# Performance work log

Measured on AMD Instinct MI355X. Metric: run time of the kernel, lower is better.

The kernel has to match this reference:

```python
import jax, jax.numpy as jnp
import numpy as np

B, L, E = 16, 1022, 1280
D, H, FF, NL = 512, 8, 2048, 4
DH = D // H
EPS = 1e-5


def layer_norm(x, s, b):
    m = jnp.mean(x, axis=-1, keepdims=True)
    v = jnp.mean(jnp.square(x - m), axis=-1, keepdims=True)
    return (x - m) * jax.lax.rsqrt(v + EPS) * s + b


def setup_inputs() -> dict:
    key = jax.random.key(0)
    ks = jax.random.split(key, 12)
    s = 0.02
    return {
        "embeddings": jax.random.normal(ks[0], (B, L, E), jnp.float32),
        "mask": jnp.ones((B, L), jnp.float32),
        "position": jnp.tile(jnp.arange(L, dtype=jnp.int32)[None, :], (B, 1)),
        "proj_w": jax.random.normal(ks[1], (D, E), jnp.float32) * s,
        "proj_b": jnp.zeros((D,), jnp.float32),
        "proj_ln_s": jnp.ones((D,), jnp.float32),
        "proj_ln_b": jnp.zeros((D,), jnp.float32),
        "ln1_s": jnp.ones((NL, D), jnp.float32),
        "ln1_b": jnp.zeros((NL, D), jnp.float32),
        "in_w": jax.random.normal(ks[2], (NL, 3 * D, D), jnp.float32) * s,
        "in_b": jnp.zeros((NL, 3 * D), jnp.float32),
        "out_w": jax.random.normal(ks[3], (NL, D, D), jnp.float32) * s,
        "out_b": jnp.zeros((NL, D), jnp.float32),
        "ln2_s": jnp.ones((NL, D), jnp.float32),
        "ln2_b": jnp.zeros((NL, D), jnp.float32),
        "w1": jax.random.normal(ks[4], (NL, FF, D), jnp.float32) * s,
        "b1": jnp.zeros((NL, FF), jnp.float32),
        "w2": jax.random.normal(ks[5], (NL, D, FF), jnp.float32) * s,
        "b2": jnp.zeros((NL, D), jnp.float32),
        "h1_w": jax.random.normal(ks[6], (128, 2 * D), jnp.float32) * s,
        "h1_b": jnp.zeros((128,), jnp.float32),
        "hln_s": jnp.ones((128,), jnp.float32),
        "hln_b": jnp.zeros((128,), jnp.float32),
        "h2_w": jax.random.normal(ks[7], (1, 128), jnp.float32) * s,
        "h2_b": jnp.zeros((1,), jnp.float32),
    }


def _rope_tables():
    inv_freq = 1.0 / (10000.0 ** (jnp.arange(0, DH, 2, dtype=jnp.float32) / DH))
    t = jnp.arange(L, dtype=jnp.float32)
    freqs = jnp.outer(t, inv_freq)          # [L, DH/2]
    emb = jnp.concatenate([freqs, freqs], axis=-1)  # [L, DH]
    return jnp.cos(emb), jnp.sin(emb)


def _rotate_half(x):
    x1, x2 = jnp.split(x, 2, axis=-1)
    return jnp.concatenate([-x2, x1], axis=-1)


def _apply_rope(x, cos, sin):
    # x: [B, L, D] -> per-head rotation -> [B, L, D]
    xh = x.reshape(B, L, H, DH)
    xh = xh * cos[None, :, None, :] + _rotate_half(xh) * sin[None, :, None, :]
    return xh.reshape(B, L, D)


def _forward(embeddings, mask, proj_w, proj_b, proj_ln_s, proj_ln_b,
             ln1_s, ln1_b, in_w, in_b, out_w, out_b, ln2_s, ln2_b,
             w1, b1, w2, b2, h1_w, h1_b, hln_s, hln_b, h2_w, h2_b):
    cos, sin = _rope_tables()
    x = layer_norm(embeddings @ proj_w.T + proj_b, proj_ln_s, proj_ln_b)  # [B,L,D]
    pad = mask <= 0  # True where padded (~mask.bool())
    scale = 1.0 / jnp.sqrt(jnp.float32(DH))
    for i in range(NL):
        n = layer_norm(x, ln1_s[i], ln1_b[i])
        q_in = _apply_rope(n, cos, sin)
        k_in = _apply_rope(n, cos, sin)
        v_in = n
        wq, wk, wv = jnp.split(in_w[i], 3, axis=0)
        bq, bk, bv = jnp.split(in_b[i], 3, axis=0)
        qh = (q_in @ wq.T + bq).reshape(B, L, H, DH)
        kh = (k_in @ wk.T + bk).reshape(B, L, H, DH)
        vh = (v_in @ wv.T + bv).reshape(B, L, H, DH)
        scores = jnp.einsum('blhd,bmhd->bhlm', qh, kh) * scale
        scores = jnp.where(pad[:, None, None, :], jnp.float32(-1e9), scores)
        attn = jax.nn.softmax(scores, axis=-1)
        o = jnp.einsum('bhlm,bmhd->blhd', attn, vh).reshape(B, L, D)
        x = x + (o @ out_w[i].T + out_b[i])
        n2 = layer_norm(x, ln2_s[i], ln2_b[i])
        x = x + (jax.nn.relu(n2 @ w1[i].T + b1[i]) @ w2[i].T + b2[i])
    # masked mean pool
    gctx = (x * mask[..., None]).sum(axis=1) / mask.sum(axis=1, keepdims=True)  # [B,D]
    combined = jnp.concatenate([x, jnp.broadcast_to(gctx[:, None, :], (B, L, D))], axis=-1)
    h = jax.nn.relu(layer_norm(combined @ h1_w.T + h1_b, hln_s, hln_b))
    logits = (h @ h2_w.T + h2_b).squeeze(-1)  # [B,L]
    return logits


def reference(embeddings, mask, position, proj_w, proj_b, proj_ln_s, proj_ln_b,
              ln1_s, ln1_b, in_w, in_b, out_w, out_b, ln2_s, ln2_b,
              w1, b1, w2, b2, h1_w, h1_b, hln_s, hln_b, h2_w, h2_b):
    # position is accepted for API parity but unused (as in the torch module)
    return _forward(embeddings, mask, proj_w, proj_b, proj_ln_s, proj_ln_b,
                    ln1_s, ln1_b, in_w, in_b, out_w, out_b, ln2_s, ln2_b,
                    w1, b1, w2, b2, h1_w, h1_b, hln_s, hln_b, h2_w, h2_b)
```

## Files before the change

kernel.cpp:

```cpp
#include <hip/hip_runtime.h>
#include <cstdint>
#include <cstddef>

#define B_   16
#define L_   1022
#define E_   1280
#define D_   512
#define H_   8
#define FF_  2048
#define NL_  4
#define DH_  64
#define BL_  (B_*L_)
#define EPS_ 1e-5f

typedef unsigned short u16;
typedef unsigned int   u32;
typedef unsigned long long u64;
typedef float f32x4 __attribute__((ext_vector_type(4)));
typedef short s16x8 __attribute__((ext_vector_type(8)));
typedef u32 u32x4 __attribute__((ext_vector_type(4)));

__device__ __forceinline__ u16 f2bf(float f) {
    u32 u = __builtin_bit_cast(u32, f);
    u += 0x7fffu + ((u >> 16) & 1u);
    return (u16)(u >> 16);
}
__device__ __forceinline__ float bf2f(u16 u) {
    return __builtin_bit_cast(float, (u32)u << 16);
}
__device__ __forceinline__ u32 pack2bf(float a, float b) {
    return (u32)f2bf(a) | ((u32)f2bf(b) << 16);
}

__global__ __launch_bounds__(256)
void cast_k(const float* __restrict__ src, u16* __restrict__ dst, int n8) {
    int t = blockIdx.x * 256 + threadIdx.x;
    if (t >= n8) return;
    const float* s = src + (size_t)t * 8;
    float4 a = *(const float4*)(s);
    float4 b = *(const float4*)(s + 4);
    s16x8 o;
    o[0] = (short)f2bf(a.x); o[1] = (short)f2bf(a.y);
    o[2] = (short)f2bf(a.z); o[3] = (short)f2bf(a.w);
    o[4] = (short)f2bf(b.x); o[5] = (short)f2bf(b.y);
    o[6] = (short)f2bf(b.z); o[7] = (short)f2bf(b.w);
    *(s16x8*)(dst + (size_t)t * 8) = o;
}

__global__ __launch_bounds__(256)
void h1cast_k(const float* __restrict__ src, u16* __restrict__ dst) {
    int t = blockIdx.x * 256 + threadIdx.x;
    if (t >= 128 * 512 / 8) return;
    int row = t >> 6, c8 = (t & 63) << 3;
    const float* s = src + (size_t)row * 1024 + c8;
    float4 a = *(const float4*)(s);
    float4 b = *(const float4*)(s + 4);
    s16x8 o;
    o[0] = (short)f2bf(a.x); o[1] = (short)f2bf(a.y);
    o[2] = (short)f2bf(a.z); o[3] = (short)f2bf(a.w);
    o[4] = (short)f2bf(b.x); o[5] = (short)f2bf(b.y);
    o[6] = (short)f2bf(b.z); o[7] = (short)f2bf(b.w);
    *(s16x8*)(dst + (size_t)row * 512 + c8) = o;
}

__global__ void tables_k(float* __restrict__ ct, float* __restrict__ st) {
    int idx = blockIdx.x * blockDim.x + threadIdx.x;
    if (idx >= L_ * DH_) return;
    int l = idx / DH_;
    int d = idx % DH_;
    int j = d & 31;
    float invf = powf(10000.0f, -(float)(2 * j) / (float)DH_);
    float ang = (float)l * invf;
    ct[idx] = cosf(ang);
    st[idx] = sinf(ang);
}

template<bool RELU, bool RESID, bool OUTBF, bool ROWBIAS>
__global__ __launch_bounds__(256)
void mgemm_k(const u16* __restrict__ A, const u16* __restrict__ W,
             const float* __restrict__ bias, const float* __restrict__ resid,
             void* __restrict__ Cout, int M, int N, int K)
{
    constexpr int LDT = 72;
    __shared__ u16 As[128 * LDT];
    __shared__ u16 Ws[128 * LDT];
    const int nt = N >> 7;
    const int bx = blockIdx.x % nt;
    const int by = blockIdx.x / nt;
    const int m0 = by << 7, n0 = bx << 7;
    const int tid = threadIdx.x;
    const int lane = tid & 63, wid = tid >> 6;
    const int wr = wid >> 1, wc = wid & 1;
    const int lr = lane & 15, lk = lane >> 4;

    f32x4 acc[4][4];
#pragma unroll
    for (int m = 0; m < 4; m++)
#pragma unroll
        for (int n = 0; n < 4; n++) acc[m][n] = (f32x4)0.0f;

    for (int k0 = 0; k0 < K; k0 += 64) {
        s16x8 va[4], vw[4];
#pragma unroll
        for (int u = 0; u < 4; u++) {
            int ch = tid + (u << 8);
            int r = ch >> 3, c8 = (ch & 7) << 3;
            int ar = m0 + r; if (ar >= M) ar = M - 1;
            va[u] = *(const s16x8*)(A + (size_t)ar * K + k0 + c8);
            vw[u] = *(const s16x8*)(W + (size_t)(n0 + r) * K + k0 + c8);
        }
        __syncthreads();
#pragma unroll
        for (int u = 0; u < 4; u++) {
            int ch = tid + (u << 8);
            int r = ch >> 3, c8 = (ch & 7) << 3;
            *(s16x8*)&As[r * LDT + c8] = va[u];
            *(s16x8*)&Ws[r * LDT + c8] = vw[u];
        }
        __syncthreads();
#pragma unroll
        for (int kk = 0; kk < 2; kk++) {
            s16x8 af[4], bf[4];
#pragma unroll
            for (int m = 0; m < 4; m++)
                af[m] = *(const s16x8*)&As[(wr * 64 + m * 16 + lr) * LDT + kk * 32 + lk * 8];
#pragma unroll
            for (int n = 0; n < 4; n++)
                bf[n] = *(const s16x8*)&Ws[(wc * 64 + n * 16 + lr) * LDT + kk * 32 + lk * 8];
#pragma unroll
            for (int m = 0; m < 4; m++)
#pragma unroll
                for (int n = 0; n < 4; n++)
                    acc[m][n] = __builtin_amdgcn_mfma_f32_16x16x32_bf16(
                        af[m], bf[n], acc[m][n], 0, 0, 0);
        }
    }

    float bv[4];
    if constexpr (!ROWBIAS) {
#pragma unroll
        for (int n = 0; n < 4; n++) bv[n] = bias[n0 + wc * 64 + n * 16 + lr];
    }
#pragma unroll
    for (int m = 0; m < 4; m++) {
#pragma unroll
        for (int j = 0; j < 4; j++) {
            int row = m0 + wr * 64 + m * 16 + lk * 4 + j;
            if (row >= M) continue;
            const float* rb = nullptr;
            if constexpr (ROWBIAS) rb = bias + (size_t)(row / L_) * N;
#pragma unroll
            for (int n = 0; n < 4; n++) {
                int col = n0 + wc * 64 + n * 16 + lr;
                float c = acc[m][n][j];
                if constexpr (ROWBIAS) c += rb[col];
                else                   c += bv[n];
                if constexpr (RELU) c = fmaxf(c, 0.0f);
                if constexpr (RESID) c += resid[(size_t)row * N + col];
                if constexpr (OUTBF) ((u16*)Cout)[(size_t)row * N + col] = f2bf(c);
                else                 ((float*)Cout)[(size_t)row * N + col] = c;
            }
        }
    }
}

template<int DD, bool RELU, bool OUTBF>
__global__ __launch_bounds__(256)
void ln_k(const float* __restrict__ x, const float* __restrict__ s,
          const float* __restrict__ bb, void* __restrict__ out, int M)
{
    const int lane = threadIdx.x & 63;
    const int row = (blockIdx.x << 2) + (threadIdx.x >> 6);
    if (row >= M) return;
    const float* xr = x + (size_t)row * DD;
    constexpr int NV = DD / 64;
    float v[NV];
    if constexpr (NV == 8) {
        *(float4*)(v)     = *(const float4*)(xr + lane * 8);
        *(float4*)(v + 4) = *(const float4*)(xr + lane * 8 + 4);
    } else {
        float2 t = *(const float2*)(xr + lane * 2);
        v[0] = t.x; v[1] = t.y;
    }
    float sum = 0.f, sq = 0.f;
#pragma unroll
    for (int e = 0; e < NV; e++) { sum += v[e]; sq += v[e] * v[e]; }
#pragma unroll
    for (int msk = 1; msk < 64; msk <<= 1) {
        sum += __shfl_xor(sum, msk);
        sq  += __shfl_xor(sq, msk);
    }
    const float mean = sum * (1.0f / DD);
    const float var  = sq * (1.0f / DD) - mean * mean;
    const float rstd = rsqrtf(var + EPS_);
#pragma unroll
    for (int e = 0; e < NV; e++) {
        int d = lane * NV + e;
        float r = (v[e] - mean) * rstd * s[d] + bb[d];
        if constexpr (RELU) r = fmaxf(r, 0.0f);
        v[e] = r;
    }
    if constexpr (OUTBF) {
        u16* orow = (u16*)out + (size_t)row * DD;
        if constexpr (NV == 8) {
            s16x8 o;
#pragma unroll
            for (int e = 0; e < 8; e++) o[e] = (short)f2bf(v[e]);
            *(s16x8*)(orow + lane * 8) = o;
        } else {
            orow[lane * 2] = f2bf(v[0]); orow[lane * 2 + 1] = f2bf(v[1]);
        }
    } else {
        float* orow = (float*)out + (size_t)row * DD;
        if constexpr (NV == 8) {
            *(float4*)(orow + lane * 8)     = *(float4*)(v);
            *(float4*)(orow + lane * 8 + 4) = *(float4*)(v + 4);
        } else {
            float2 t; t.x = v[0]; t.y = v[1];
            *(float2*)(orow + lane * 2) = t;
        }
    }
}

__global__ __launch_bounds__(256)
void rope_k(const u16* __restrict__ n, const float* __restrict__ ct,
            const float* __restrict__ st, u16* __restrict__ r)
{
    int t = blockIdx.x * 256 + threadIdx.x;
    if (t >= BL_ * D_ / 8) return;
    int idx = t << 3;
    int l = (idx / D_) % L_;
    int d = idx & (D_ - 1);
    int dd = d & 63;
    s16x8 xv = *(const s16x8*)(n + idx);
    int pidx; float sgn;
    if (dd < 32) { pidx = idx + 32; sgn = -1.0f; }
    else         { pidx = idx - 32; sgn =  1.0f; }
    s16x8 pv = *(const s16x8*)(n + pidx);
    float4 c0 = *(const float4*)(ct + l * DH_ + dd);
    float4 c1 = *(const float4*)(ct + l * DH_ + dd + 4);
    float4 s0 = *(const float4*)(st + l * DH_ + dd);
    float4 s1 = *(const float4*)(st + l * DH_ + dd + 4);
    float cc[8] = {c0.x,c0.y,c0.z,c0.w,c1.x,c1.y,c1.z,c1.w};
    float ss[8] = {s0.x,s0.y,s0.z,s0.w,s1.x,s1.y,s1.z,s1.w};
    s16x8 o;
#pragma unroll
    for (int e = 0; e < 8; e++) {
        float xf = bf2f((u16)xv[e]);
        float pf = bf2f((u16)pv[e]);
        o[e] = (short)f2bf(xf * cc[e] + sgn * pf * ss[e]);
    }
    *(s16x8*)(r + idx) = o;
}

__global__ __launch_bounds__(256)
void attn_k(const u16* __restrict__ qk, const u16* __restrict__ v,
            const float* __restrict__ mask, u16* __restrict__ o)
{
    constexpr int LDA = 68;
    __shared__ u16 Kt[64 * LDA];
    __shared__ u16 Vt[64 * LDA];
    const int bh = blockIdx.x >> 4, qt = blockIdx.x & 15;
    const int b = bh >> 3, h = bh & 7;
    const int tid = threadIdx.x;
    const int lane = tid & 63, w = tid >> 6;
    const int lr = lane & 15, lg = lane >> 4;
    const size_t basebl = (size_t)b * L_;

    const int qrow = qt * 64 + w * 16 + lr;
    const int qc = qrow < L_ ? qrow : L_ - 1;
    s16x8 bq[2];
#pragma unroll
    for (int kk = 0; kk < 2; kk++)
        bq[kk] = *(const s16x8*)(qk + (basebl + qc) * 1024 + h * DH_ + kk * 32 + lg * 8);

    f32x4 oacc[4];
#pragma unroll
    for (int n = 0; n < 4; n++) oacc[n] = (f32x4)0.0f;
    float m_run = -1e30f, l_run = 0.f;

    const int st_key = tid >> 3;
    const int st_d8 = (tid & 7) << 3;
    const int src0 = lr + ((lane & 16) << 1);
    const int src1 = src0 + 16;
    const bool ahi = (lg >> 1) != 0;

    for (int kt = 0; kt < 16; kt++) {
        __syncthreads();
#pragma unroll
        for (int u = 0; u < 2; u++) {
            int key = st_key + u * 32;
            int gk = kt * 64 + key; if (gk >= L_) gk = L_ - 1;
            s16x8 kv = *(const s16x8*)(qk + (basebl + gk) * 1024 + 512 + h * DH_ + st_d8);
            s16x8 vv = *(const s16x8*)(v  + (basebl + gk) * D_ + h * DH_ + st_d8);
            *(s16x8*)&Kt[key * LDA + st_d8] = kv;
#pragma unroll
            for (int e = 0; e < 8; e++) Vt[(st_d8 + e) * LDA + key] = (u16)vv[e];
        }
        __syncthreads();

        int gkey = kt * 64 + lane;
        bool vb = (gkey < L_) && (mask[basebl + gkey] > 0.0f);
        u64 vm = __ballot(vb);

        f32x4 sacc[4];
#pragma unroll
        for (int n = 0; n < 4; n++) {
            sacc[n] = (f32x4)0.0f;
#pragma unroll
            for (int kk = 0; kk < 2; kk++) {
                s16x8 ak = *(const s16x8*)&Kt[(n * 16 + lr) * LDA + kk * 32 + lg * 8];
                sacc[n] = __builtin_amdgcn_mfma_f32_16x16x32_bf16(ak, bq[kk], sacc[n], 0, 0, 0);
            }
        }

        float p[4][4];
        float tm = -1e30f;
#pragma unroll
        for (int n = 0; n < 4; n++)
#pragma unroll
            for (int j = 0; j < 4; j++) {
                int kl = 16 * n + 4 * lg + j;
                float s = ((vm >> kl) & 1ull) ? sacc[n][j] * 0.125f : -1e30f;
                p[n][j] = s;
                tm = fmaxf(tm, s);
            }
        tm = fmaxf(tm, __shfl_xor(tm, 16));
        tm = fmaxf(tm, __shfl_xor(tm, 32));
        float nm = fmaxf(m_run, tm);
        float corr = __expf(m_run - nm);
        m_run = nm;
        float ts = 0.f;
#pragma unroll
        for (int n = 0; n < 4; n++)
#pragma unroll
            for (int j = 0; j < 4; j++) {
                p[n][j] = __expf(p[n][j] - nm);
                ts += p[n][j];
            }
        ts += __shfl_xor(ts, 16);
        ts += __shfl_xor(ts, 32);
        l_run = l_run * corr + ts;
#pragma unroll
        for (int n = 0; n < 4; n++) oacc[n] *= corr;

        u32 pk[4][2];
#pragma unroll
        for (int n = 0; n < 4; n++) {
            pk[n][0] = pack2bf(p[n][0], p[n][1]);
            pk[n][1] = pack2bf(p[n][2], p[n][3]);
        }
        u32 r0[4][2], r1[4][2];
#pragma unroll
        for (int n = 0; n < 4; n++)
#pragma unroll
            for (int i = 0; i < 2; i++) {
                r0[n][i] = (u32)__shfl((int)pk[n][i], src0);
                r1[n][i] = (u32)__shfl((int)pk[n][i], src1);
            }
#pragma unroll
        for (int kk = 0; kk < 2; kk++) {
            u32x4 bw;
            bw[0] = ahi ? r0[2 * kk + 1][0] : r0[2 * kk][0];
            bw[1] = ahi ? r0[2 * kk + 1][1] : r0[2 * kk][1];
            bw[2] = ahi ? r1[2 * kk + 1][0] : r1[2 * kk][0];
            bw[3] = ahi ? r1[2 * kk + 1][1] : r1[2 * kk][1];
            s16x8 bp = __builtin_bit_cast(s16x8, bw);
#pragma unroll
            for (int n2 = 0; n2 < 4; n2++) {
                s16x8 av = *(const s16x8*)&Vt[(n2 * 16 + lr) * LDA + kk * 32 + lg * 8];
                oacc[n2] = __builtin_amdgcn_mfma_f32_16x16x32_bf16(av, bp, oacc[n2], 0, 0, 0);
            }
        }
    }

    __syncthreads();
    u16* Ol = &Kt[w * 16 * LDA];
    float inv = 1.0f / l_run;
#pragma unroll
    for (int n = 0; n < 4; n++)
#pragma unroll
        for (int j = 0; j < 4; j++)
            Ol[lr * LDA + 16 * n + 4 * lg + j] = f2bf(oacc[n][j] * inv);
    int orow = lane >> 2, oc = (lane & 3) * 16;
    int qg = qt * 64 + w * 16 + orow;
    if (qg < L_) {
        s16x8 o0 = *(const s16x8*)&Ol[orow * LDA + oc];
        s16x8 o1 = *(const s16x8*)&Ol[orow * LDA + oc + 8];
        *(s16x8*)(o + (basebl + qg) * D_ + h * DH_ + oc) = o0;
        *(s16x8*)(o + (basebl + qg) * D_ + h * DH_ + oc + 8) = o1;
    }
}

__global__ __launch_bounds__(512)
void pool1_k(const float* __restrict__ x, const float* __restrict__ mask,
             float* __restrict__ pp, float* __restrict__ mp)
{
    const int b = blockIdx.x, sp = blockIdx.y;
    const int d = threadIdx.x;
    const int l0 = sp * 64;
    float acc = 0.f;
    for (int l = l0; l < l0 + 64 && l < L_; l++)
        acc += x[((size_t)b * L_ + l) * D_ + d] * mask[b * L_ + l];
    pp[((size_t)b * 16 + sp) * D_ + d] = acc;
    if (d == 0) {
        float ms = 0.f;
        for (int l = l0; l < l0 + 64 && l < L_; l++) ms += mask[b * L_ + l];
        mp[b * 16 + sp] = ms;
    }
}

__global__ __launch_bounds__(512)
void pool2_k(const float* __restrict__ pp, const float* __restrict__ mp,
             float* __restrict__ g)
{
    const int b = blockIdx.x;
    const int d = threadIdx.x;
    float acc = 0.f, ms = 0.f;
#pragma unroll
    for (int sp = 0; sp < 16; sp++) {
        acc += pp[((size_t)b * 16 + sp) * D_ + d];
        ms += mp[b * 16 + sp];
    }
    g[b * D_ + d] = acc / ms;
}

__global__ __launch_bounds__(256)
void gpart_k(const float* __restrict__ g, const float* __restrict__ h1w,
             const float* __restrict__ h1b, float* __restrict__ gp)
{
    const int lane = threadIdx.x & 63;
    const int gid = (blockIdx.x << 2) + (threadIdx.x >> 6);
    const int b = gid >> 7, j = gid & 127;
    const float* wr = h1w + (size_t)j * (2 * D_) + D_;
    const float* gr = g + b * D_;
    float4 a0 = *(const float4*)(gr + lane * 8);
    float4 a1 = *(const float4*)(gr + lane * 8 + 4);
    float4 w0 = *(const float4*)(wr + lane * 8);
    float4 w1v = *(const float4*)(wr + lane * 8 + 4);
    float acc = a0.x * w0.x + a0.y * w0.y + a0.z * w0.z + a0.w * w0.w
              + a1.x * w1v.x + a1.y * w1v.y + a1.z * w1v.z + a1.w * w1v.w;
#pragma unroll
    for (int msk = 1; msk < 64; msk <<= 1) acc += __shfl_xor(acc, msk);
    if (lane == 0) gp[b * 128 + j] = acc + h1b[j];
}

__global__ __launch_bounds__(256)
void logits_k(const float* __restrict__ h, const float* __restrict__ w,
              const float* __restrict__ bsc, float* __restrict__ out, int M)
{
    const int lane = threadIdx.x & 63;
    const int row = (blockIdx.x << 2) + (threadIdx.x >> 6);
    if (row >= M) return;
    float2 hv = *(const float2*)(h + (size_t)row * 128 + lane * 2);
    float2 wv = *(const float2*)(w + lane * 2);
    float acc = hv.x * wv.x + hv.y * wv.y;
#pragma unroll
    for (int msk = 1; msk < 64; msk <<= 1) acc += __shfl_xor(acc, msk);
    if (lane == 0) out[row] = acc + bsc[0];
}

extern "C" void kernel_launch(void* const* d_in, const int* in_sizes, int n_in,
                              void* d_out, int out_size, void* d_ws, size_t ws_size,
                              hipStream_t stream)
{
    const float* emb       = (const float*)d_in[0];
    const float* mask      = (const float*)d_in[1];
    const float* proj_w    = (const float*)d_in[3];
    const float* proj_b    = (const float*)d_in[4];
    const float* proj_ln_s = (const float*)d_in[5];
    const float* proj_ln_b = (const float*)d_in[6];
    const float* ln1_s     = (const float*)d_in[7];
    const float* ln1_b     = (const float*)d_in[8];
    const float* in_w      = (const float*)d_in[9];
    const float* in_b      = (const float*)d_in[10];
    const float* out_w     = (const float*)d_in[11];
    const float* out_b     = (const float*)d_in[12];
    const float* ln2_s     = (const float*)d_in[13];
    const float* ln2_b     = (const float*)d_in[14];
    const float* w1        = (const float*)d_in[15];
    const float* b1        = (const float*)d_in[16];
    const float* w2        = (const float*)d_in[17];
    const float* b2        = (const float*)d_in[18];
    const float* h1_w      = (const float*)d_in[19];
    const float* h1_b      = (const float*)d_in[20];
    const float* hln_s     = (const float*)d_in[21];
    const float* hln_b     = (const float*)d_in[22];
    const float* h2_w      = (const float*)d_in[23];
    const float* h2_b      = (const float*)d_in[24];
    float* out = (float*)d_out;

    float* ws = (float*)d_ws;
    const size_t S = (size_t)BL_ * D_;
    float* X  = ws;
    float* Rf = ws + S;
    u16* QKB   = (u16*)(ws + S);
    u16* VB    = (u16*)(ws + 2 * S);
    u16* NbB   = (u16*)(ws + 2 * S) + S;
    u16* FFb16 = (u16*)(ws + 3 * S);
    u16* RopeB = FFb16;
    u16* embB  = FFb16;
    u16* RB    = (u16*)(ws + 4 * S);
    u16* projwB = (u16*)(ws + 5 * S);
    u16* iwB  = projwB + 512 * 1280;
    u16* owB  = iwB + (size_t)NL_ * 3 * D_ * D_;
    u16* w1B  = owB + (size_t)NL_ * D_ * D_;
    u16* w2B  = w1B + (size_t)NL_ * FF_ * D_;
    u16* h1wB = w2B + (size_t)NL_ * D_ * FF_;
    float* CT = ws + 5 * S + 6651904;
    float* ST = CT + L_ * DH_;
    float* GC = ST + L_ * DH_;
    float* GP = GC + B_ * D_;
    float* Pp = GP + B_ * 128;
    float* Mp = Pp + (size_t)B_ * 16 * D_;
    float* Hb = Rf;

    const int MT = 128;
    const dim3 blk(256);
    const int lnGrid = (BL_ + 3) / 4;

    cast_k<<<(BL_ * E_ / 8 + 255) / 256, blk, 0, stream>>>(emb, embB, BL_ * E_ / 8);
    cast_k<<<(512 * 1280 / 8 + 255) / 256, blk, 0, stream>>>(proj_w, projwB, 512 * 1280 / 8);
    cast_k<<<(NL_ * 3 * D_ * D_ / 8 + 255) / 256, blk, 0, stream>>>(in_w, iwB, NL_ * 3 * D_ * D_ / 8);
    cast_k<<<(NL_ * D_ * D_ / 8 + 255) / 256, blk, 0, stream>>>(out_w, owB, NL_ * D_ * D_ / 8);
    cast_k<<<(NL_ * FF_ * D_ / 8 + 255) / 256, blk, 0, stream>>>(w1, w1B, NL_ * FF_ * D_ / 8);
    cast_k<<<(NL_ * D_ * FF_ / 8 + 255) / 256, blk, 0, stream>>>(w2, w2B, NL_ * D_ * FF_ / 8);
    h1cast_k<<<(128 * 512 / 8 + 255) / 256, blk, 0, stream>>>(h1_w, h1wB);
    tables_k<<<(L_ * DH_ + 255) / 256, blk, 0, stream>>>(CT, ST);

    mgemm_k<false,false,false,false><<<MT * (D_ / 128), blk, 0, stream>>>(
        embB, projwB, proj_b, nullptr, Rf, BL_, D_, E_);
    ln_k<D_,false,false><<<lnGrid, blk, 0, stream>>>(Rf, proj_ln_s, proj_ln_b, X, BL_);

    for (int i = 0; i < NL_; i++) {
        const u16* iw = iwB + (size_t)i * 3 * D_ * D_;
        const float* ib = in_b + (size_t)i * 3 * D_;
        ln_k<D_,false,true><<<lnGrid, blk, 0, stream>>>(X, ln1_s + i * D_, ln1_b + i * D_, NbB, BL_);
        mgemm_k<false,false,true,false><<<MT * 4, blk, 0, stream>>>(
            NbB, iw + 2 * D_ * D_, ib + 2 * D_, nullptr, VB, BL_, D_, D_);
        rope_k<<<(BL_ * D_ / 8 + 255) / 256, blk, 0, stream>>>(NbB, CT, ST, RopeB);
        mgemm_k<false,false,true,false><<<MT * 8, blk, 0, stream>>>(
            RopeB, iw, ib, nullptr, QKB, BL_, 1024, D_);
        attn_k<<<B_ * H_ * 16, blk, 0, stream>>>(QKB, VB, mask, RB);
        mgemm_k<false,true,false,false><<<MT * 4, blk, 0, stream>>>(
            RB, owB + (size_t)i * D_ * D_, out_b + i * D_, X, X, BL_, D_, D_);
        ln_k<D_,false,true><<<lnGrid, blk, 0, stream>>>(X, ln2_s + i * D_, ln2_b + i * D_, NbB, BL_);
        mgemm_k<true,false,true,false><<<MT * 16, blk, 0, stream>>>(
            NbB, w1B + (size_t)i * FF_ * D_, b1 + i * FF_, nullptr, FFb16, BL_, FF_, D_);
        mgemm_k<false,true,false,false><<<MT * 4, blk, 0, stream>>>(
            FFb16, w2B + (size_t)i * D_ * FF_, b2 + i * D_, X, X, BL_, D_, FF_);
    }

    pool1_k<<<dim3(B_, 16), dim3(512), 0, stream>>>(X, mask, Pp, Mp);
    pool2_k<<<B_, dim3(512), 0, stream>>>(Pp, Mp, GC);
    gpart_k<<<(B_ * 128) / 4, blk, 0, stream>>>(GC, h1_w, h1_b, GP);
    cast_k<<<(int)((S / 8 + 255) / 256), blk, 0, stream>>>(X, NbB, (int)(S / 8));
    mgemm_k<false,false,false,true><<<MT * 1, blk, 0, stream>>>(
        NbB, h1wB, GP, nullptr, Hb, BL_, 128, D_);
    ln_k<128,true,false><<<lnGrid, blk, 0, stream>>>(Hb, hln_s, hln_b, Hb, BL_);
    logits_k<<<lnGrid, blk, 0, stream>>>(Hb, h2_w, h2_b, out, BL_);
}
```

Before: 1.468 ms.

## Double-buffer attention K/V tiles, fold softmax scale into Q weights, lazy rescale

The attention kernel now double-buffers its K/V shared-memory tiles, staging the next tile while computing the current one, which removes one barrier per iteration. The 1/sqrt(dh)*log2(e) factor is folded into the Q projection weights and bias at cast time, so softmax uses exp2f with no per-score multiply. The running-max rescale of the output accumulator is skipped unless the max grows by more than a threshold. Costs are double the shared memory (lower occupancy) and a small bf16 rounding change from pre-scaling the weights.

After: 1.501 ms. 2.2% more time.

```diff
diff --git a/kernel.cpp b/kernel.cpp
--- a/kernel.cpp
+++ b/kernel.cpp
@@ -12,6 +12,7 @@
 #define DH_  64
 #define BL_  (B_*L_)
 #define EPS_ 1e-5f
+#define QSC_ 0.18033688011112042f
 
 typedef unsigned short u16;
 typedef unsigned int   u32;
@@ -45,6 +46,32 @@
     o[4] = (short)f2bf(b.x); o[5] = (short)f2bf(b.y);
     o[6] = (short)f2bf(b.z); o[7] = (short)f2bf(b.w);
     *(s16x8*)(dst + (size_t)t * 8) = o;
+}
+
+__global__ __launch_bounds__(256)
+void castq_k(const float* __restrict__ src, u16* __restrict__ dst, int n8) {
+    int t = blockIdx.x * 256 + threadIdx.x;
+    if (t >= n8) return;
+    int row = t >> 6;
+    float sc = (row % 1536) < 512 ? QSC_ : 1.0f;
+    const float* s = src + (size_t)t * 8;
+    float4 a = *(const float4*)(s);
+    float4 b = *(const float4*)(s + 4);
+    s16x8 o;
+    o[0] = (short)f2bf(a.x * sc); o[1] = (short)f2bf(a.y * sc);
+    o[2] = (short)f2bf(a.z * sc); o[3] = (short)f2bf(a.w * sc);
+    o[4] = (short)f2bf(b.x * sc); o[5] = (short)f2bf(b.y * sc);
+    o[6] = (short)f2bf(b.z * sc); o[7] = (short)f2bf(b.w * sc);
+    *(s16x8*)(dst + (size_t)t * 8) = o;
+}
+
+__global__ __launch_bounds__(256)
+void qbias_k(const float* __restrict__ ib, float* __restrict__ qbs) {
+    int t = blockIdx.x * 256 + threadIdx.x;
+    if (t >= NL_ * 1024) return;
+    int i = t >> 10, j = t & 1023;
+    float sc = j < 512 ? QSC_ : 1.0f;
+    qbs[t] = ib[i * 1536 + j] * sc;
 }
 
 __global__ __launch_bounds__(256)
@@ -258,8 +285,9 @@
             const float* __restrict__ mask, u16* __restrict__ o)
 {
     constexpr int LDA = 68;
-    __shared__ u16 Kt[64 * LDA];
-    __shared__ u16 Vt[64 * LDA];
+    constexpr int TSZ = 64 * LDA;
+    __shared__ u16 Kt[2 * TSZ];
+    __shared__ u16 Vt[2 * TSZ];
     const int bh = blockIdx.x >> 4, qt = blockIdx.x & 15;
     const int b = bh >> 3, h = bh & 7;
     const int tid = threadIdx.x;
@@ -285,19 +313,26 @@
     const int src1 = src0 + 16;
     const bool ahi = (lg >> 1) != 0;
 
-    for (int kt = 0; kt < 16; kt++) {
-        __syncthreads();
+    auto stage = [&](int buf, int kt_) {
 #pragma unroll
         for (int u = 0; u < 2; u++) {
             int key = st_key + u * 32;
-            int gk = kt * 64 + key; if (gk >= L_) gk = L_ - 1;
+            int gk = kt_ * 64 + key; if (gk >= L_) gk = L_ - 1;
             s16x8 kv = *(const s16x8*)(qk + (basebl + gk) * 1024 + 512 + h * DH_ + st_d8);
             s16x8 vv = *(const s16x8*)(v  + (basebl + gk) * D_ + h * DH_ + st_d8);
-            *(s16x8*)&Kt[key * LDA + st_d8] = kv;
-#pragma unroll
-            for (int e = 0; e < 8; e++) Vt[(st_d8 + e) * LDA + key] = (u16)vv[e];
-        }
-        __syncthreads();
+            *(s16x8*)&Kt[buf * TSZ + key * LDA + st_d8] = kv;
+#pragma unroll
+            for (int e = 0; e < 8; e++)
+                Vt[buf * TSZ + (st_d8 + e) * LDA + key] = (u16)vv[e];
+        }
+    };
+
+    stage(0, 0);
+    __syncthreads();
+
+    for (int kt = 0; kt < 16; kt++) {
+        const int cur = kt & 1;
+        if (kt < 15) stage(cur ^ 1, kt + 1);
 
         int gkey = kt * 64 + lane;
         bool vb = (gkey < L_) && (mask[basebl + gkey] > 0.0f);
@@ -309,7 +344,7 @@
             sacc[n] = (f32x4)0.0f;
 #pragma unroll
             for (int kk = 0; kk < 2; kk++) {
-                s16x8 ak = *(const s16x8*)&Kt[(n * 16 + lr) * LDA + kk * 32 + lg * 8];
+                s16x8 ak = *(const s16x8*)&Kt[cur * TSZ + (n * 16 + lr) * LDA + kk * 32 + lg * 8];
                 sacc[n] = __builtin_amdgcn_mfma_f32_16x16x32_bf16(ak, bq[kk], sacc[n], 0, 0, 0);
             }
         }
@@ -321,28 +356,31 @@
 #pragma unroll
             for (int j = 0; j < 4; j++) {
                 int kl = 16 * n + 4 * lg + j;
-                float s = ((vm >> kl) & 1ull) ? sacc[n][j] * 0.125f : -1e30f;
+                float s = ((vm >> kl) & 1ull) ? sacc[n][j] : -1e30f;
                 p[n][j] = s;
                 tm = fmaxf(tm, s);
             }
         tm = fmaxf(tm, __shfl_xor(tm, 16));
         tm = fmaxf(tm, __shfl_xor(tm, 32));
-        float nm = fmaxf(m_run, tm);
-        float corr = __expf(m_run - nm);
-        m_run = nm;
+        if (!__all(tm - m_run <= 8.0f)) {
+            float nm = fmaxf(m_run, tm);
+            float corr = exp2f(m_run - nm);
+            l_run *= corr;
+#pragma unroll
+            for (int n = 0; n < 4; n++) oacc[n] *= corr;
+            m_run = nm;
+        }
         float ts = 0.f;
 #pragma unroll
         for (int n = 0; n < 4; n++)
 #pragma unroll
             for (int j = 0; j < 4; j++) {
-                p[n][j] = __expf(p[n][j] - nm);
+                p[n][j] = exp2f(p[n][j] - m_run);
                 ts += p[n][j];
             }
         ts += __shfl_xor(ts, 16);
         ts += __shfl_xor(ts, 32);
-        l_run = l_run * corr + ts;
-#pragma unroll
-        for (int n = 0; n < 4; n++) oacc[n] *= corr;
+        l_run += ts;
 
         u32 pk[4][2];
 #pragma unroll
@@ -368,13 +406,13 @@
             s16x8 bp = __builtin_bit_cast(s16x8, bw);
 #pragma unroll
             for (int n2 = 0; n2 < 4; n2++) {
-                s16x8 av = *(const s16x8*)&Vt[(n2 * 16 + lr) * LDA + kk * 32 + lg * 8];
+                s16x8 av = *(const s16x8*)&Vt[cur * TSZ + (n2 * 16 + lr) * LDA + kk * 32 + lg * 8];
                 oacc[n2] = __builtin_amdgcn_mfma_f32_16x16x32_bf16(av, bp, oacc[n2], 0, 0, 0);
             }
         }
-    }
-
-    __syncthreads();
+        __syncthreads();
+    }
+
     u16* Ol = &Kt[w * 16 * LDA];
     float inv = 1.0f / l_run;
 #pragma unroll
@@ -513,6 +551,7 @@
     float* GP = GC + B_ * D_;
     float* Pp = GP + B_ * 128;
     float* Mp = Pp + (size_t)B_ * 16 * D_;
+    float* QBS = Mp + B_ * 16;
     float* Hb = Rf;
 
     const int MT = 128;
@@ -521,7 +560,8 @@
 
     cast_k<<<(BL_ * E_ / 8 + 255) / 256, blk, 0, stream>>>(emb, embB, BL_ * E_ / 8);
     cast_k<<<(512 * 1280 / 8 + 255) / 256, blk, 0, stream>>>(proj_w, projwB, 512 * 1280 / 8);
-    cast_k<<<(NL_ * 3 * D_ * D_ / 8 + 255) / 256, blk, 0, stream>>>(in_w, iwB, NL_ * 3 * D_ * D_ / 8);
+    castq_k<<<(NL_ * 3 * D_ * D_ / 8 + 255) / 256, blk, 0, stream>>>(in_w, iwB, NL_ * 3 * D_ * D_ / 8);
+    qbias_k<<<(NL_ * 1024 + 255) / 256, blk, 0, stream>>>(in_b, QBS);
     cast_k<<<(NL_ * D_ * D_ / 8 + 255) / 256, blk, 0, stream>>>(out_w, owB, NL_ * D_ * D_ / 8);
     cast_k<<<(NL_ * FF_ * D_ / 8 + 255) / 256, blk, 0, stream>>>(w1, w1B, NL_ * FF_ * D_ / 8);
     cast_k<<<(NL_ * D_ * FF_ / 8 + 255) / 256, blk, 0, stream>>>(w2, w2B, NL_ * D_ * FF_ / 8);
@@ -540,7 +580,7 @@
             NbB, iw + 2 * D_ * D_, ib + 2 * D_, nullptr, VB, BL_, D_, D_);
         rope_k<<<(BL_ * D_ / 8 + 255) / 256, blk, 0, stream>>>(NbB, CT, ST, RopeB);
         mgemm_k<false,false,true,false><<<MT * 8, blk, 0, stream>>>(
-            RopeB, iw, ib, nullptr, QKB, BL_, 1024, D_);
+            RopeB, iw, QBS + (size_t)i * 1024, nullptr, QKB, BL_, 1024, D_);
         attn_k<<<B_ * H_ * 16, blk, 0, stream>>>(QKB, VB, mask, RB);
         mgemm_k<false,true,false,false><<<MT * 4, blk, 0, stream>>>(
             RB, owB + (size_t)i * D_ * D_, out_b + i * D_, X, X, BL_, D_, D_);
```
